# Optimization experiments

Hardware: AMD Instinct MI355X
Metric: run time of the kernel (lower is better)

The kernel has to match this reference:

```python
import jax, jax.numpy as jnp
import numpy as np

T, N, E = 4, 50000, 800000
F_IN, H, O, C = 128, 128, 128, 2


def setup_inputs() -> dict:
    key = jax.random.key(0)
    ks = jax.random.split(key, 9)
    s = 0.05
    return {
        "graph": jax.random.randint(ks[0], (T, 2, E), 0, N),
        "fts": jax.random.normal(ks[1], (T, N, F_IN), dtype=jnp.float32),
        "time_steps": T,
        # SAGEConv 1: lin_l (aggregated, has bias) and lin_r (root)
        "W1l": jax.random.normal(ks[2], (H, F_IN), dtype=jnp.float32) * s,
        "b1": jnp.zeros((H,), dtype=jnp.float32),
        "W1r": jax.random.normal(ks[3], (H, F_IN), dtype=jnp.float32) * s,
        # SAGEConv 2
        "W2l": jax.random.normal(ks[4], (O, H), dtype=jnp.float32) * s,
        "b2": jnp.zeros((O,), dtype=jnp.float32),
        "W2r": jax.random.normal(ks[5], (O, H), dtype=jnp.float32) * s,
        # final classifier Linear(out_channels, nclass)
        "Wc": jax.random.normal(ks[6], (C, O), dtype=jnp.float32) * s,
        "bc": jnp.zeros((C,), dtype=jnp.float32),
    }


def sage_conv(x, src, dst, Wl, bl, Wr, n_nodes):
    # PyG SAGEConv(aggr='mean'): out = lin_l(mean_{j->i} x_j) + lin_r(x_i)
    msg = x[src]                                                # [E, F] gather
    summed = jax.ops.segment_sum(msg, dst, num_segments=n_nodes)
    cnt = jax.ops.segment_sum(jnp.ones((src.shape[0], 1), x.dtype), dst,
                              num_segments=n_nodes)
    mean = summed / jnp.maximum(cnt, 1.0)                       # [N, F]
    return mean @ Wl.T + bl + x @ Wr.T


def reference(graph, fts, time_steps, W1l, b1, W1r, W2l, b2, W2r, Wc, bc):
    n = fts.shape[1]
    # per-time-step first SAGEConv with that step's graph
    def step(x_t, ei_t):
        return jax.nn.leaky_relu(
            sage_conv(x_t, ei_t[0], ei_t[1], W1l, b1, W1r, n), 0.2)
    ys = jax.vmap(step)(fts, graph)                             # [T, N, H]
    # last SAGEConv applied to the stacked tensor with the LAST graph (as in source)
    ei = graph[-1]
    y2 = jax.vmap(lambda y: sage_conv(y, ei[0], ei[1], W2l, b2, W2r, n))(ys)
    y2 = jax.nn.leaky_relu(y2, 0.2)                             # [T, N, O]
    logits = y2 @ Wc.T + bc                                     # [T, N, C]
    out = jax.nn.log_softmax(logits, axis=1)                    # softmax over node dim (as in source)
    return out.reshape(n, -1)                                   # [N, T*C]
```

## Files before the change

### kernel.cpp

```cpp
#include <hip/hip_runtime.h>
#include <hip/hip_bf16.h>

#define TT 4
#define FD 128
#define CC 2
#define LSE_CH 32
#define WROW 264

#define NPB 64
#define NPB_SHIFT 6
#define NBUKMAX 1024
#define CAP 1536
#define BIN_TILE 2048

typedef __attribute__((ext_vector_type(8))) short bf16x8;
typedef __attribute__((ext_vector_type(4))) float f32x4;
typedef __attribute__((ext_vector_type(4))) float fvec4;

__device__ __forceinline__ float bf2f(unsigned int h) {
    union { unsigned int u; float f; } v; v.u = h << 16; return v.f;
}
__device__ __forceinline__ unsigned short f2bf(float f) {
    union { float f; unsigned int u; } v; v.f = f;
    unsigned int u = v.u;
    unsigned int r = u + 0x7FFFu + ((u >> 16) & 1u);
    return (unsigned short)(r >> 16);
}
__device__ __forceinline__ unsigned int pack2(float lo, float hi) {
    return ((unsigned int)f2bf(hi) << 16) | (unsigned int)f2bf(lo);
}
__device__ __forceinline__ void add8(float* a, uint4 v) {
    a[0] += bf2f(v.x & 0xFFFF); a[1] += bf2f(v.x >> 16);
    a[2] += bf2f(v.y & 0xFFFF); a[3] += bf2f(v.y >> 16);
    a[4] += bf2f(v.z & 0xFFFF); a[5] += bf2f(v.z >> 16);
    a[6] += bf2f(v.w & 0xFFFF); a[7] += bf2f(v.w >> 16);
}
__device__ __forceinline__ fvec4 ntld_f4(const float* p) {
    return __builtin_nontemporal_load((const fvec4*)p);
}


__global__ __launch_bounds__(256)
void bin_kernel(const int* __restrict__ graph, int* __restrict__ gcount,
                unsigned int* __restrict__ bdata, int e, int nbuk) {
    int g = blockIdx.y;
    const int* src = graph + (size_t)g * 2 * e;
    const int* dst = src + e;
    int tbeg = blockIdx.x * BIN_TILE;
    __shared__ int cnt[NBUKMAX];
    __shared__ int base[NBUKMAX];
    for (int i = threadIdx.x; i < nbuk; i += 256) cnt[i] = 0;

    int d[8], s[8];
    bool valid[8];
    #pragma unroll
    for (int u = 0; u < 8; ++u) {
        int i = tbeg + u * 256 + threadIdx.x;
        valid[u] = i < e;
        if (valid[u]) { d[u] = dst[i]; s[u] = src[i]; }
    }
    __syncthreads();
    #pragma unroll
    for (int u = 0; u < 8; ++u)
        if (valid[u]) atomicAdd(&cnt[d[u] >> NPB_SHIFT], 1);
    __syncthreads();
    for (int i = threadIdx.x; i < nbuk; i += 256) {
        int c = cnt[i];
        base[i] = (c > 0) ? atomicAdd(&gcount[g * nbuk + i], c) : 0;
        cnt[i] = 0;
    }
    __syncthreads();
    #pragma unroll
    for (int u = 0; u < 8; ++u) {
        if (valid[u]) {
            int b = d[u] >> NPB_SHIFT;
            int pos = base[b] + atomicAdd(&cnt[b], 1);
            if (pos < CAP)
                bdata[((size_t)g * nbuk + b) * CAP + pos] =
                    ((unsigned int)(d[u] & (NPB - 1)) << 16) | (unsigned int)s[u];
        }
    }
}

__global__ __launch_bounds__(1024)
void bucket_scan_kernel(const int* __restrict__ gcount, int* __restrict__ bbase, int nbuk) {
    int g = blockIdx.x;
    __shared__ int sm[1024];
    int v = (threadIdx.x < nbuk) ? gcount[g * nbuk + threadIdx.x] : 0;
    sm[threadIdx.x] = v;
    __syncthreads();
    #pragma unroll
    for (int off = 1; off < 1024; off <<= 1) {
        int t = (threadIdx.x >= off) ? sm[threadIdx.x - off] : 0;
        __syncthreads();
        sm[threadIdx.x] += t;
        __syncthreads();
    }
    if (threadIdx.x < nbuk) bbase[g * nbuk + threadIdx.x] = sm[threadIdx.x] - v;
}

__global__ __launch_bounds__(256)
void build_kernel(const unsigned int* __restrict__ bdata, const int* __restrict__ gcount,
                  const int* __restrict__ bbase, int* __restrict__ arr,
                  unsigned short* __restrict__ col, int n, int nbuk, int e) {
    int g = blockIdx.y;
    int b = blockIdx.x;
    int M = gcount[g * nbuk + b];
    if (M > CAP) M = CAP;
    int base = bbase[g * nbuk + b];
    const unsigned int* rec = bdata + ((size_t)g * nbuk + b) * CAP;
    __shared__ int deg[NPB];
    __shared__ int cursor[NPB];
    if (threadIdx.x < NPB) deg[threadIdx.x] = 0;
    __syncthreads();
    for (int i = threadIdx.x; i < M; i += 256)
        atomicAdd(&deg[rec[i] >> 16], 1);
    __syncthreads();
    if (threadIdx.x < NPB) {
        int d = deg[threadIdx.x];
        int incl = d;
        #pragma unroll
        for (int off = 1; off < NPB; off <<= 1) {
            int t = __shfl_up(incl, off, 64);
            if ((int)threadIdx.x >= off) incl += t;
        }
        cursor[threadIdx.x] = base + incl - d;
        int node = b * NPB + threadIdx.x;
        if (node < n) arr[(size_t)g * n + node] = base + incl;
    }
    __syncthreads();
    for (int i = threadIdx.x; i < M; i += 256) {
        unsigned int r = rec[i];
        int p = atomicAdd(&cursor[r >> 16], 1);
        if (p < e) col[(size_t)g * e + p] = (unsigned short)(r & 0xFFFF);
    }
}


__global__ __launch_bounds__(256)
void conv_kernel(const float* __restrict__ fts, unsigned short* __restrict__ xT, int total8) {
    int tid = blockIdx.x * 256 + threadIdx.x;
    if (tid >= total8) return;
    const float* s = fts + (size_t)tid * 8;
    fvec4 a = ntld_f4(s);
    fvec4 b = ntld_f4(s + 4);
    uint4 o;
    o.x = pack2(a[0], a[1]); o.y = pack2(a[2], a[3]);
    o.z = pack2(b[0], b[1]); o.w = pack2(b[2], b[3]);
    *(uint4*)(xT + (size_t)tid * 8) = o;
}

__global__ void pack_weights_kernel(const float* __restrict__ W1l, const float* __restrict__ W1r,
                                    const float* __restrict__ W2l, const float* __restrict__ W2r,
                                    unsigned short* __restrict__ o1, unsigned short* __restrict__ o2) {
    int i = blockIdx.x * blockDim.x + threadIdx.x;
    if (i >= 128 * 256) return;
    const float* Wl = blockIdx.y ? W2l : W1l;
    const float* Wr = blockIdx.y ? W2r : W1r;
    unsigned short* out = blockIdx.y ? o2 : o1;
    int j = i >> 8, k = i & 255;
    float v = (k < 128) ? Wl[j * 128 + k] : Wr[j * 128 + (k - 128)];
    out[i] = f2bf(v);
}


__global__ __launch_bounds__(256)
void agg_kernel(const int* __restrict__ arr, const unsigned short* __restrict__ col,
                const unsigned short* __restrict__ x, unsigned short* __restrict__ mean,
                int n) {
    int node = (blockIdx.x << 2) + (threadIdx.x >> 6);
    if (node >= n) return;
    int lane = threadIdx.x & 63;
    int eg = lane >> 4;
    int fl = lane & 15;
    int beg = (node == 0) ? 0 : arr[node - 1];
    int end = arr[node];
    float acc[8] = {0.f, 0.f, 0.f, 0.f, 0.f, 0.f, 0.f, 0.f};
    const unsigned short* xb = x + fl * 8;
    int e = beg;
    while (e + 32 <= end) {
        uint4 v[8];
        #pragma unroll
        for (int u = 0; u < 8; ++u)
            v[u] = *(const uint4*)(xb + (size_t)col[e + 4 * u + eg] * FD);
        #pragma unroll
        for (int u = 0; u < 8; ++u) add8(acc, v[u]);
        e += 32;
    }
    if (e < end) {
        uint4 v[8];
        bool p[8];
        #pragma unroll
        for (int u = 0; u < 8; ++u) {
            int idx = e + 4 * u + eg;
            p[u] = idx < end;
            if (p[u]) v[u] = *(const uint4*)(xb + (size_t)col[idx] * FD);
        }
        #pragma unroll
        for (int u = 0; u < 8; ++u)
            if (p[u]) add8(acc, v[u]);
    }
    #pragma unroll
    for (int j = 0; j < 8; ++j) {
        acc[j] += __shfl_xor(acc[j], 16);
        acc[j] += __shfl_xor(acc[j], 32);
    }
    if (eg == 0) {
        int deg = end - beg;
        float inv = 1.f / (float)(deg > 1 ? deg : 1);
        uint4 o;
        o.x = pack2(acc[0] * inv, acc[1] * inv);
        o.y = pack2(acc[2] * inv, acc[3] * inv);
        o.z = pack2(acc[4] * inv, acc[5] * inv);
        o.w = pack2(acc[6] * inv, acc[7] * inv);
        *(uint4*)(mean + (size_t)node * FD + fl * 8) = o;
    }
}


__global__ __launch_bounds__(256, 2)
void sage_gemm_kernel(const unsigned short* Am, const unsigned short* __restrict__ Ax,
                      const unsigned short* __restrict__ Wcat, const float* __restrict__ bias,
                      unsigned short* out, int mrows) {
    int wave = threadIdx.x >> 6;
    int lane = threadIdx.x & 63;
    int m = lane & 15, q = lane >> 4;
    int rowBase = blockIdx.x * 256 + wave * 64;

    int arow[4];
    #pragma unroll
    for (int g = 0; g < 4; ++g) {
        int r = rowBase + g * 16 + m;
        arow[g] = (r < mrows) ? r : (mrows - 1);
    }

    bf16x8 af[3][4];
    #pragma unroll
    for (int g = 0; g < 4; ++g)
        af[0][g] = *(const bf16x8*)(Am + (size_t)arow[g] * FD + 0 * 32 + q * 8);
    #pragma unroll
    for (int g = 0; g < 4; ++g)
        af[1][g] = *(const bf16x8*)(Am + (size_t)arow[g] * FD + 1 * 32 + q * 8);

    __shared__ unsigned short Wlds[128 * WROW];
    for (int i = threadIdx.x; i < 128 * 32; i += 256) {
        int row = i >> 5, seg = i & 31;
        *(uint4*)(&Wlds[row * WROW + seg * 8]) = *(const uint4*)(Wcat + row * 256 + seg * 8);
    }
    __syncthreads();

    f32x4 acc[4][8];
    #pragma unroll
    for (int g = 0; g < 4; ++g)
        #pragma unroll
        for (int ct = 0; ct < 8; ++ct) acc[g][ct] = (f32x4){0.f, 0.f, 0.f, 0.f};

    #pragma unroll
    for (int step = 0; step < 8; ++step) {
        if (step < 6) {
            const unsigned short* An = (step + 2 < 4) ? Am : Ax;
            int kan = ((step + 2) & 3) * 32 + q * 8;
            #pragma unroll
            for (int g = 0; g < 4; ++g)
                af[(step + 2) % 3][g] = *(const bf16x8*)(An + (size_t)arow[g] * FD + kan);
        }
        int kw = step * 32 + q * 8;
        bf16x8 bfrag[8];
        #pragma unroll
        for (int ct = 0; ct < 8; ++ct)
            bfrag[ct] = *(const bf16x8*)(&Wlds[(ct * 16 + m) * WROW + kw]);
        #pragma unroll
        for (int g = 0; g < 4; ++g)
            #pragma unroll
            for (int ct = 0; ct < 8; ++ct)
                acc[g][ct] = __builtin_amdgcn_mfma_f32_16x16x32_bf16(af[step % 3][g], bfrag[ct], acc[g][ct], 0, 0, 0);
    }

    #pragma unroll
    for (int g = 0; g < 4; ++g) {
        #pragma unroll
        for (int ct = 0; ct < 8; ++ct) {
            int colc = ct * 16 + m;
            float b = bias[colc];
            #pragma unroll
            for (int r = 0; r < 4; ++r) {
                int row = rowBase + g * 16 + q * 4 + r;
                if (row < mrows) {
                    float v = acc[g][ct][r] + b;
                    v = (v >= 0.f) ? v : 0.2f * v;
                    out[(size_t)row * FD + colc] = f2bf(v);
                }
            }
        }
    }
}


__global__ __launch_bounds__(256, 2)
void gemm2_cls_kernel(const unsigned short* __restrict__ Am, const unsigned short* __restrict__ Ax,
                      const unsigned short* __restrict__ Wcat, const float* __restrict__ bias,
                      const float* __restrict__ Wc, const float* __restrict__ bc,
                      float* __restrict__ logits, int mrows) {
    int wave = threadIdx.x >> 6;
    int lane = threadIdx.x & 63;
    int m = lane & 15, q = lane >> 4;
    int rowBase = blockIdx.x * 256 + wave * 64;

    int arow[4];
    #pragma unroll
    for (int g = 0; g < 4; ++g) {
        int r = rowBase + g * 16 + m;
        arow[g] = (r < mrows) ? r : (mrows - 1);
    }

    bf16x8 af[3][4];
    #pragma unroll
    for (int g = 0; g < 4; ++g)
        af[0][g] = *(const bf16x8*)(Am + (size_t)arow[g] * FD + 0 * 32 + q * 8);
    #pragma unroll
    for (int g = 0; g < 4; ++g)
        af[1][g] = *(const bf16x8*)(Am + (size_t)arow[g] * FD + 1 * 32 + q * 8);

    __shared__ unsigned short Wlds[128 * WROW];
    for (int i = threadIdx.x; i < 128 * 32; i += 256) {
        int row = i >> 5, seg = i & 31;
        *(uint4*)(&Wlds[row * WROW + seg * 8]) = *(const uint4*)(Wcat + row * 256 + seg * 8);
    }
    __syncthreads();

    f32x4 acc[4][8];
    #pragma unroll
    for (int g = 0; g < 4; ++g)
        #pragma unroll
        for (int ct = 0; ct < 8; ++ct) acc[g][ct] = (f32x4){0.f, 0.f, 0.f, 0.f};

    #pragma unroll
    for (int step = 0; step < 8; ++step) {
        if (step < 6) {
            const unsigned short* An = (step + 2 < 4) ? Am : Ax;
            int kan = ((step + 2) & 3) * 32 + q * 8;
            #pragma unroll
            for (int g = 0; g < 4; ++g)
                af[(step + 2) % 3][g] = *(const bf16x8*)(An + (size_t)arow[g] * FD + kan);
        }
        int kw = step * 32 + q * 8;
        bf16x8 bfrag[8];
        #pragma unroll
        for (int ct = 0; ct < 8; ++ct)
            bfrag[ct] = *(const bf16x8*)(&Wlds[(ct * 16 + m) * WROW + kw]);
        #pragma unroll
        for (int g = 0; g < 4; ++g)
            #pragma unroll
            for (int ct = 0; ct < 8; ++ct)
                acc[g][ct] = __builtin_amdgcn_mfma_f32_16x16x32_bf16(af[step % 3][g], bfrag[ct], acc[g][ct], 0, 0, 0);
    }

    float wc0[8], wc1[8], bb[8];
    #pragma unroll
    for (int ct = 0; ct < 8; ++ct) {
        wc0[ct] = Wc[ct * 16 + m];
        wc1[ct] = Wc[FD + ct * 16 + m];
        bb[ct]  = bias[ct * 16 + m];
    }
    float bc0 = bc[0], bc1 = bc[1];

    #pragma unroll
    for (int g = 0; g < 4; ++g) {
        #pragma unroll
        for (int r = 0; r < 4; ++r) {
            float p0 = 0.f, p1 = 0.f;
            #pragma unroll
            for (int ct = 0; ct < 8; ++ct) {
                float v = acc[g][ct][r] + bb[ct];
                v = (v >= 0.f) ? v : 0.2f * v;
                p0 += v * wc0[ct];
                p1 += v * wc1[ct];
            }
            #pragma unroll
            for (int off = 8; off > 0; off >>= 1) {
                p0 += __shfl_down(p0, off);
                p1 += __shfl_down(p1, off);
            }
            if (m == 0) {
                int row = rowBase + g * 16 + q * 4 + r;
                if (row < mrows) {
                    size_t base = (size_t)row * CC;
                    logits[base]     = p0 + bc0;
                    logits[base + 1] = p1 + bc1;
                }
            }
        }
    }
}


__global__ __launch_bounds__(256)
void lse_partial_kernel(const float* __restrict__ logits, float* __restrict__ pm,
                        float* __restrict__ ps, int n) {
    int tc = blockIdx.y;
    int t = tc >> 1, c = tc & 1;
    const float* p = logits + (size_t)t * n * CC + c;
    float m = -1e30f, s = 0.f;
    for (int i = blockIdx.x * 256 + threadIdx.x; i < n; i += LSE_CH * 256) {
        float v = p[(size_t)i * CC];
        if (v > m) { s = s * __expf(m - v) + 1.f; m = v; }
        else s += __expf(v - m);
    }
    __shared__ float smm[256], sms[256];
    smm[threadIdx.x] = m; sms[threadIdx.x] = s;
    __syncthreads();
    for (int off = 128; off > 0; off >>= 1) {
        if (threadIdx.x < off) {
            float m2 = smm[threadIdx.x + off], s2 = sms[threadIdx.x + off];
            float M = fmaxf(smm[threadIdx.x], m2);
            sms[threadIdx.x] = sms[threadIdx.x] * __expf(smm[threadIdx.x] - M) + s2 * __expf(m2 - M);
            smm[threadIdx.x] = M;
        }
        __syncthreads();
    }
    if (threadIdx.x == 0) { pm[tc * LSE_CH + blockIdx.x] = smm[0]; ps[tc * LSE_CH + blockIdx.x] = sms[0]; }
}

__global__ __launch_bounds__(256)
void sub_lse_kernel(const float* __restrict__ logits, const float* __restrict__ pm,
                    const float* __restrict__ ps, float* __restrict__ out, int total, int n) {
    __shared__ float slse[8];
    int tc = threadIdx.x >> 5;
    int l32 = threadIdx.x & 31;
    float m = pm[tc * LSE_CH + l32];
    float s = ps[tc * LSE_CH + l32];
    #pragma unroll
    for (int off = 16; off > 0; off >>= 1) {
        float m2 = __shfl_down(m, off, 32);
        float s2 = __shfl_down(s, off, 32);
        float M = fmaxf(m, m2);
        s = s * __expf(m - M) + s2 * __expf(m2 - M);
        m = M;
    }
    if (l32 == 0) slse[tc] = m + logf(s);
    __syncthreads();
    int i = blockIdx.x * 256 + threadIdx.x;
    if (i < total) {
        int c = i & 1;
        int t = i / (n * CC);
        out[i] = logits[i] - slse[t * CC + c];
    }
}


extern "C" void kernel_launch(void* const* d_in, const int* in_sizes, int n_in,
                              void* d_out, int out_size, void* d_ws, size_t ws_size,
                              hipStream_t stream) {
    const int* graph = (const int*)d_in[0];
    const float* fts = (const float*)d_in[1];
    const float* W1l = (const float*)d_in[3];
    const float* b1  = (const float*)d_in[4];
    const float* W1r = (const float*)d_in[5];
    const float* W2l = (const float*)d_in[6];
    const float* b2  = (const float*)d_in[7];
    const float* W2r = (const float*)d_in[8];
    const float* Wc  = (const float*)d_in[9];
    const float* bc  = (const float*)d_in[10];
    float* out = (float*)d_out;

    const int T = TT;
    const int E = in_sizes[0] / (T * 2);
    const int N = in_sizes[1] / (T * FD);
    const int NBUK = (N + NPB - 1) >> NPB_SHIFT;

    size_t off = 0;
    auto alloc = [&](size_t bytes) -> char* {
        char* p = (char*)d_ws + off;
        off += (bytes + 511) & ~(size_t)511;
        return p;
    };
    int* arr_all = (int*)alloc((size_t)T * N * 4);
    unsigned short* col_all = (unsigned short*)alloc((size_t)T * E * 2);
    int* gcount = (int*)alloc((size_t)T * NBUK * 4);
    int* bbase  = (int*)alloc((size_t)T * NBUK * 4);
    unsigned short* wcat1 = (unsigned short*)alloc(128 * 256 * 2);
    unsigned short* wcat2 = (unsigned short*)alloc(128 * 256 * 2);
    float* logits = (float*)alloc((size_t)T * N * CC * 4);
    float* pm  = (float*)alloc((size_t)T * CC * LSE_CH * 4);
    float* ps  = (float*)alloc((size_t)T * CC * LSE_CH * 4);
    unsigned short* R1 = (unsigned short*)alloc((size_t)T * N * FD * 2);
    unsigned short* R2 = (unsigned short*)alloc((size_t)T * N * FD * 2);
    unsigned int* bdata = (unsigned int*)R1;
    unsigned short* xT = R1;
    unsigned short* mean2T = R1;
    unsigned short* mean1T = R2;
    unsigned short* ysT = R2;

    dim3 pwgrid((128 * 256 + 255) / 256, 2);
    pack_weights_kernel<<<pwgrid, 256, 0, stream>>>(W1l, W1r, W2l, W2r, wcat1, wcat2);

    hipMemsetAsync(gcount, 0, (size_t)T * NBUK * 4, stream);
    dim3 bingrid((E + BIN_TILE - 1) / BIN_TILE, T);
    bin_kernel<<<bingrid, 256, 0, stream>>>(graph, gcount, bdata, E, NBUK);
    bucket_scan_kernel<<<T, 1024, 0, stream>>>(gcount, bbase, NBUK);
    dim3 buildgrid(NBUK, T);
    build_kernel<<<buildgrid, 256, 0, stream>>>(bdata, gcount, bbase, arr_all, col_all, N, NBUK, E);

    int total8 = T * N * 16;
    conv_kernel<<<(total8 + 255) / 256, 256, 0, stream>>>(fts, xT, total8);

    int aggblocks = (N + 3) / 4;
    for (int t = 0; t < T; ++t)
        agg_kernel<<<aggblocks, 256, 0, stream>>>(arr_all + (size_t)t * N,
                                                  col_all + (size_t)t * E,
                                                  xT + (size_t)t * N * FD,
                                                  mean1T + (size_t)t * N * FD, N);
    int mrows = T * N;
    sage_gemm_kernel<<<(mrows + 255) / 256, 256, 0, stream>>>(mean1T, xT, wcat1, b1, ysT, mrows);

    const int* arrL = arr_all + (size_t)(T - 1) * N;
    const unsigned short* colL = col_all + (size_t)(T - 1) * E;
    for (int t = 0; t < T; ++t)
        agg_kernel<<<aggblocks, 256, 0, stream>>>(arrL, colL,
                                                  ysT + (size_t)t * N * FD,
                                                  mean2T + (size_t)t * N * FD, N);
    gemm2_cls_kernel<<<(mrows + 255) / 256, 256, 0, stream>>>(mean2T, ysT, wcat2, b2,
                                                              Wc, bc, logits, mrows);

    dim3 lgrid(LSE_CH, T * CC);
    lse_partial_kernel<<<lgrid, 256, 0, stream>>>(logits, pm, ps, N);
    int total = T * N * CC;
    sub_lse_kernel<<<(total + 255) / 256, 256, 0, stream>>>(logits, pm, ps, out, total, N);
}
```

Before: 567.2 us.

## Fuse binning with fp32-to-bf16 conversion, drop bucket scan, batch aggregation launches

Merges the edge-binning and feature-conversion kernels into one launch, which needs a dedicated bdata buffer instead of aliasing R1. It removes the separate bucket-scan kernel by having each build block reduce the preceding bucket counts itself. The per-time-step aggregation loops become single launches covering all time steps. The aim is fewer kernel launches and serial dependencies, paid for with redundant prefix-sum reads in build_kernel and extra workspace memory.

Measured after the change: 530.2 us. 6.5% less time.

```diff
diff --git a/kernel.cpp b/kernel.cpp
--- a/kernel.cpp
+++ b/kernel.cpp
@@ -41,14 +41,28 @@
 
 
 __global__ __launch_bounds__(256)
-void bin_kernel(const int* __restrict__ graph, int* __restrict__ gcount,
-                unsigned int* __restrict__ bdata, int e, int nbuk) {
-    int g = blockIdx.y;
+void prep_kernel(const int* __restrict__ graph, int* __restrict__ gcount,
+                 unsigned int* __restrict__ bdata, int e, int nbuk, int bpg, int binBlocks,
+                 const float* __restrict__ fts, unsigned short* __restrict__ xT, int total8) {
+    __shared__ int cnt[NBUKMAX];
+    __shared__ int base[NBUKMAX];
+    if ((int)blockIdx.x >= binBlocks) {
+        int tid = (blockIdx.x - binBlocks) * 256 + threadIdx.x;
+        if (tid >= total8) return;
+        const float* s = fts + (size_t)tid * 8;
+        fvec4 a = ntld_f4(s);
+        fvec4 b = ntld_f4(s + 4);
+        uint4 o;
+        o.x = pack2(a[0], a[1]); o.y = pack2(a[2], a[3]);
+        o.z = pack2(b[0], b[1]); o.w = pack2(b[2], b[3]);
+        *(uint4*)(xT + (size_t)tid * 8) = o;
+        return;
+    }
+    int g = blockIdx.x / bpg;
+    int bx = blockIdx.x - g * bpg;
     const int* src = graph + (size_t)g * 2 * e;
     const int* dst = src + e;
-    int tbeg = blockIdx.x * BIN_TILE;
-    __shared__ int cnt[NBUKMAX];
-    __shared__ int base[NBUKMAX];
+    int tbeg = bx * BIN_TILE;
     for (int i = threadIdx.x; i < nbuk; i += 256) cnt[i] = 0;
 
     int d[8], s[8];
@@ -82,32 +96,27 @@
     }
 }
 
-__global__ __launch_bounds__(1024)
-void bucket_scan_kernel(const int* __restrict__ gcount, int* __restrict__ bbase, int nbuk) {
-    int g = blockIdx.x;
-    __shared__ int sm[1024];
-    int v = (threadIdx.x < nbuk) ? gcount[g * nbuk + threadIdx.x] : 0;
-    sm[threadIdx.x] = v;
-    __syncthreads();
-    #pragma unroll
-    for (int off = 1; off < 1024; off <<= 1) {
-        int t = (threadIdx.x >= off) ? sm[threadIdx.x - off] : 0;
-        __syncthreads();
-        sm[threadIdx.x] += t;
-        __syncthreads();
-    }
-    if (threadIdx.x < nbuk) bbase[g * nbuk + threadIdx.x] = sm[threadIdx.x] - v;
-}
 
 __global__ __launch_bounds__(256)
 void build_kernel(const unsigned int* __restrict__ bdata, const int* __restrict__ gcount,
-                  const int* __restrict__ bbase, int* __restrict__ arr,
-                  unsigned short* __restrict__ col, int n, int nbuk, int e) {
+                  int* __restrict__ arr, unsigned short* __restrict__ col,
+                  int n, int nbuk, int e) {
     int g = blockIdx.y;
     int b = blockIdx.x;
     int M = gcount[g * nbuk + b];
     if (M > CAP) M = CAP;
-    int base = bbase[g * nbuk + b];
+    __shared__ int red[256];
+    int pre = 0;
+    for (int i = threadIdx.x; i < b; i += 256) pre += gcount[g * nbuk + i];
+    red[threadIdx.x] = pre;
+    __syncthreads();
+    #pragma unroll
+    for (int off = 128; off > 0; off >>= 1) {
+        if (threadIdx.x < off) red[threadIdx.x] += red[threadIdx.x + off];
+        __syncthreads();
+    }
+    int base = red[0];
+
     const unsigned int* rec = bdata + ((size_t)g * nbuk + b) * CAP;
     __shared__ int deg[NPB];
     __shared__ int cursor[NPB];
@@ -134,20 +143,6 @@
         int p = atomicAdd(&cursor[r >> 16], 1);
         if (p < e) col[(size_t)g * e + p] = (unsigned short)(r & 0xFFFF);
     }
-}
-
-
-__global__ __launch_bounds__(256)
-void conv_kernel(const float* __restrict__ fts, unsigned short* __restrict__ xT, int total8) {
-    int tid = blockIdx.x * 256 + threadIdx.x;
-    if (tid >= total8) return;
-    const float* s = fts + (size_t)tid * 8;
-    fvec4 a = ntld_f4(s);
-    fvec4 b = ntld_f4(s + 4);
-    uint4 o;
-    o.x = pack2(a[0], a[1]); o.y = pack2(a[2], a[3]);
-    o.z = pack2(b[0], b[1]); o.w = pack2(b[2], b[3]);
-    *(uint4*)(xT + (size_t)tid * 8) = o;
 }
 
 __global__ void pack_weights_kernel(const float* __restrict__ W1l, const float* __restrict__ W1r,
@@ -165,11 +160,18 @@
 
 
 __global__ __launch_bounds__(256)
-void agg_kernel(const int* __restrict__ arr, const unsigned short* __restrict__ col,
-                const unsigned short* __restrict__ x, unsigned short* __restrict__ mean,
-                int n) {
-    int node = (blockIdx.x << 2) + (threadIdx.x >> 6);
+void agg_kernel(const int* __restrict__ arr0, const unsigned short* __restrict__ col0,
+                const unsigned short* __restrict__ x0, unsigned short* __restrict__ mean0,
+                int n, int bpt, int strideArr, int strideCol) {
+    int t = blockIdx.x / bpt;
+    int nb = blockIdx.x - t * bpt;
+    int node = (nb << 2) + (threadIdx.x >> 6);
     if (node >= n) return;
+    const int* arr = arr0 + (size_t)t * strideArr;
+    const unsigned short* col = col0 + (size_t)t * strideCol;
+    const unsigned short* x = x0 + (size_t)t * n * FD;
+    unsigned short* mean = mean0 + (size_t)t * n * FD;
+
     int lane = threadIdx.x & 63;
     int eg = lane >> 4;
     int fl = lane & 15;
@@ -477,15 +479,14 @@
     int* arr_all = (int*)alloc((size_t)T * N * 4);
     unsigned short* col_all = (unsigned short*)alloc((size_t)T * E * 2);
     int* gcount = (int*)alloc((size_t)T * NBUK * 4);
-    int* bbase  = (int*)alloc((size_t)T * NBUK * 4);
     unsigned short* wcat1 = (unsigned short*)alloc(128 * 256 * 2);
     unsigned short* wcat2 = (unsigned short*)alloc(128 * 256 * 2);
     float* logits = (float*)alloc((size_t)T * N * CC * 4);
     float* pm  = (float*)alloc((size_t)T * CC * LSE_CH * 4);
     float* ps  = (float*)alloc((size_t)T * CC * LSE_CH * 4);
+    unsigned int* bdata = (unsigned int*)alloc((size_t)T * NBUK * CAP * 4);
     unsigned short* R1 = (unsigned short*)alloc((size_t)T * N * FD * 2);
     unsigned short* R2 = (unsigned short*)alloc((size_t)T * N * FD * 2);
-    unsigned int* bdata = (unsigned int*)R1;
     unsigned short* xT = R1;
     unsigned short* mean2T = R1;
     unsigned short* mean1T = R2;
@@ -495,30 +496,25 @@
     pack_weights_kernel<<<pwgrid, 256, 0, stream>>>(W1l, W1r, W2l, W2r, wcat1, wcat2);
 
     hipMemsetAsync(gcount, 0, (size_t)T * NBUK * 4, stream);
-    dim3 bingrid((E + BIN_TILE - 1) / BIN_TILE, T);
-    bin_kernel<<<bingrid, 256, 0, stream>>>(graph, gcount, bdata, E, NBUK);
-    bucket_scan_kernel<<<T, 1024, 0, stream>>>(gcount, bbase, NBUK);
+
+    int bpg = (E + BIN_TILE - 1) / BIN_TILE;
+    int binBlocks = bpg * T;
+    int total8 = T * N * 16;
+    int convBlocks = (total8 + 255) / 256;
+    prep_kernel<<<binBlocks + convBlocks, 256, 0, stream>>>(
+        graph, gcount, bdata, E, NBUK, bpg, binBlocks, fts, xT, total8);
+
     dim3 buildgrid(NBUK, T);
-    build_kernel<<<buildgrid, 256, 0, stream>>>(bdata, gcount, bbase, arr_all, col_all, N, NBUK, E);
-
-    int total8 = T * N * 16;
-    conv_kernel<<<(total8 + 255) / 256, 256, 0, stream>>>(fts, xT, total8);
-
-    int aggblocks = (N + 3) / 4;
-    for (int t = 0; t < T; ++t)
-        agg_kernel<<<aggblocks, 256, 0, stream>>>(arr_all + (size_t)t * N,
-                                                  col_all + (size_t)t * E,
-                                                  xT + (size_t)t * N * FD,
-                                                  mean1T + (size_t)t * N * FD, N);
+    build_kernel<<<buildgrid, 256, 0, stream>>>(bdata, gcount, arr_all, col_all, N, NBUK, E);
+
+    int bpt = (N + 3) / 4;
+    agg_kernel<<<bpt * T, 256, 0, stream>>>(arr_all, col_all, xT, mean1T, N, bpt, N, E);
     int mrows = T * N;
     sage_gemm_kernel<<<(mrows + 255) / 256, 256, 0, stream>>>(mean1T, xT, wcat1, b1, ysT, mrows);
 
     const int* arrL = arr_all + (size_t)(T - 1) * N;
     const unsigned short* colL = col_all + (size_t)(T - 1) * E;
-    for (int t = 0; t < T; ++t)
-        agg_kernel<<<aggblocks, 256, 0, stream>>>(arrL, colL,
-                                                  ysT + (size_t)t * N * FD,
-                                                  mean2T + (size_t)t * N * FD, N);
+    agg_kernel<<<bpt * T, 256, 0, stream>>>(arrL, colL, ysT, mean2T, N, bpt, 0, 0);
     gemm2_cls_kernel<<<(mrows + 255) / 256, 256, 0, stream>>>(mean2T, ysT, wcat2, b2,
                                                               Wc, bc, logits, mrows);
 
```
